# Optimization experiments

Measured on AMD Instinct MI355X. Metric: run time of the kernel, lower is better.

## Reference

```python
import jax, jax.numpy as jnp
import numpy as np

EPS = 1e-5  # torch BatchNorm default eps


def _bn(x, gamma, beta, axes):
    # training-mode batch norm over `axes` (channel axis is 1), biased variance as in torch
    mean = x.mean(axis=axes, keepdims=True)
    var = x.var(axis=axes, keepdims=True)
    shp = [1] * x.ndim
    shp[1] = -1
    return gamma.reshape(shp) * (x - mean) * jax.lax.rsqrt(var + EPS) + beta.reshape(shp)


def setup_inputs() -> dict:
    key = jax.random.key(0)
    k0, k1, k2 = jax.random.split(key, 3)
    B, C, H, W = 4, 64, 128, 128
    OP2 = 128      # out_planes * 2
    HEAD = 8       # head_dim
    HP = OP2 // HEAD  # head_planes = 16
    return {
        "x": jax.random.normal(k0, (B, C, H, W), jnp.float32),
        "w_qkv": jax.random.normal(k1, (OP2, C), jnp.float32) / np.sqrt(C).astype(np.float32),
        "gamma1": jnp.ones((OP2,), jnp.float32),
        "beta1": jnp.zeros((OP2,), jnp.float32),
        "pos_relative": jax.random.normal(k2, (HP, 2 * H - 1), jnp.float32) / np.sqrt(C).astype(np.float32),
        "gate_qr": jnp.array([0.1], jnp.float32),
        "gate_kr": jnp.array([0.1], jnp.float32),
        "gate_v_pos": jnp.array([0.1], jnp.float32),
        "gate_v": jnp.array([1.0], jnp.float32),
        "gamma_att": jnp.ones((3 * HEAD,), jnp.float32),
        "beta_att": jnp.zeros((3 * HEAD,), jnp.float32),
        "gamma_v": jnp.ones((2 * HEAD,), jnp.float32),
        "beta_v": jnp.zeros((2 * HEAD,), jnp.float32),
    }


def reference(x, w_qkv, gamma1, beta1, pos_relative, gate_qr, gate_kr,
              gate_v_pos, gate_v, gamma_att, beta_att, gamma_v, beta_v):
    b, c, H, W = x.shape
    # h_w='h': permute [0,3,1,2] -> (b, W, c, H), fuse (b, W)
    xp = jnp.transpose(x, (0, 3, 1, 2)).reshape(b * W, c, H)  # [N, c, H]
    # to_qkv: 1x1 Conv1d (no bias) + ReLU + BatchNorm1d (training mode)
    y = jax.nn.relu(jnp.einsum('oc,ncl->nol', w_qkv, xp))      # [N, 2*out_planes, H]
    y = _bn(y, gamma1, beta1, (0, 2))

    head_dim = gamma_att.shape[0] // 3
    hp = y.shape[1] // head_dim          # head_planes
    qk_dim = hp // 4
    v_dim = hp // 2
    qkv = y.reshape(-1, head_dim, hp, H)  # [N, head_dim, head_planes, H]
    q = qkv[:, :, :qk_dim]
    k = qkv[:, :, qk_dim:2 * qk_dim]
    v = qkv[:, :, 2 * qk_dim:]

    # relative-position gather: pos_relative[:, q_idx - k_idx + H - 1] -> [head_planes, H, H]
    rel = jnp.arange(H)[:, None] - jnp.arange(H)[None, :] + H - 1
    qk_pos = pos_relative[:, rel]
    q_pos = qk_pos[:qk_dim]
    k_pos = qk_pos[qk_dim:2 * qk_dim]
    v_pos = qk_pos[2 * qk_dim:]

    qk = jnp.einsum('nhcp,nhci->nhpi', q, k)                 # [N, head_dim, H, H]
    qr = jnp.einsum('nhcp,cpi->nhpi', q, q_pos) * gate_qr
    kr = jnp.einsum('nhcp,cpi->nhpi', k, k_pos) * gate_kr

    att = _bn(jnp.concatenate([qk, qr, kr], axis=1), gamma_att, beta_att, (0, 2, 3))
    att = att.reshape(-1, 3, head_dim, H, H).sum(axis=1)
    att = jax.nn.softmax(att, axis=-1)

    att_v = jnp.einsum('nhpi,nhci->nhcp', att, v * gate_v)          # [N, head_dim, v_dim, H]
    att_vp = jnp.einsum('nhpi,cpi->nhcp', att, v_pos * gate_v_pos)

    z = _bn(jnp.concatenate([att_v, att_vp], axis=1), gamma_v, beta_v, (0, 2, 3))
    z = z.reshape(b, W, 2, head_dim * v_dim, H).sum(axis=2)  # [b, W, out_planes, H]
    # h_w='h': permute [0,2,3,1] -> (b, out_planes, H, W)
    return jnp.transpose(z, (0, 2, 3, 1))
```

## Files before the change

### kernel.cpp

```cpp
#include <hip/hip_runtime.h>
#include <hip/hip_fp16.h>

#define EPS 1e-5f



typedef _Float16 half2_t __attribute__((ext_vector_type(2)));

__device__ __constant__ int pair_c [10] = {0,0,0,0,1,1,1,2,2,3};
__device__ __constant__ int pair_cp[10] = {0,1,2,3,1,2,3,2,3,3};

__device__ inline float fdot2(half2_t a, half2_t b, float c) {
#if __has_builtin(__builtin_amdgcn_fdot2)
  return __builtin_amdgcn_fdot2(a, b, c, false);
#else
  return c + (float)a[0] * (float)b[0] + (float)a[1] * (float)b[1];
#endif
}
__device__ inline half2_t bch2(unsigned u) {
  union { unsigned u; half2_t h; } x; x.u = u; return x.h;
}
__device__ inline unsigned bcu(half2_t h) {
  union { unsigned u; half2_t h; } x; x.h = h; return x.u;
}
__device__ inline unsigned packf2(float a, float b) {
  half2_t h; h[0] = (_Float16)a; h[1] = (_Float16)b;
  union { unsigned u; half2_t h; } x; x.h = h; return x.u;
}
__device__ inline unsigned pkmul(unsigned u, half2_t c) {
  return bcu(bch2(u) * c);
}

__global__ __launch_bounds__(256) void k1_gemm(
    const float* __restrict__ x, const float* __restrict__ wq,
    _Float16* __restrict__ y1h, float* __restrict__ Pbuf)
{
  __shared__ unsigned xs[32][132];
  const int b = blockIdx.x >> 7, l = blockIdx.x & 127;
  const int tid = threadIdx.x;
  const float* xp = x + (size_t)b * 1048576 + (size_t)l * 128;
  for (int idx = tid; idx < 1024; idx += 256) {
    int cp = idx >> 5, w4 = (idx & 31) * 4;
    float4 r0 = *(const float4*)&xp[(2 * cp) * 16384 + w4];
    float4 r1 = *(const float4*)&xp[(2 * cp + 1) * 16384 + w4];
    uint4 o;
    o.x = packf2(r0.x, r1.x); o.y = packf2(r0.y, r1.y);
    o.z = packf2(r0.z, r1.z); o.w = packf2(r0.w, r1.w);
    *(uint4*)&xs[cp][w4] = o;
  }
  __syncthreads();
  const int ty = tid >> 4, tx = tid & 15;
  const int o0 = ty * 8, w0 = tx * 4;
  float acc[8][8];
#pragma unroll
  for (int u = 0; u < 8; ++u)
#pragma unroll
    for (int v = 0; v < 8; ++v) acc[u][v] = 0.f;

  for (int c4 = 0; c4 < 64; c4 += 4) {
    unsigned wr[8][2];
#pragma unroll
    for (int u = 0; u < 8; ++u) {
      float4 wv = *(const float4*)&wq[(o0 + u) * 64 + c4];
      wr[u][0] = packf2(wv.x, wv.y);
      wr[u][1] = packf2(wv.z, wv.w);
    }
    const int cp0 = c4 >> 1;
#pragma unroll
    for (int d = 0; d < 2; ++d) {
      uint4 xa = *(const uint4*)&xs[cp0 + d][w0];
      uint4 xb = *(const uint4*)&xs[cp0 + d][w0 + 64];
      half2_t a0 = bch2(xa.x), a1 = bch2(xa.y), a2 = bch2(xa.z), a3 = bch2(xa.w);
      half2_t b0 = bch2(xb.x), b1 = bch2(xb.y), b2 = bch2(xb.z), b3 = bch2(xb.w);
#pragma unroll
      for (int u = 0; u < 8; ++u) {
        half2_t wh = bch2(wr[u][d]);
        acc[u][0] = fdot2(wh, a0, acc[u][0]);
        acc[u][1] = fdot2(wh, a1, acc[u][1]);
        acc[u][2] = fdot2(wh, a2, acc[u][2]);
        acc[u][3] = fdot2(wh, a3, acc[u][3]);
        acc[u][4] = fdot2(wh, b0, acc[u][4]);
        acc[u][5] = fdot2(wh, b1, acc[u][5]);
        acc[u][6] = fdot2(wh, b2, acc[u][6]);
        acc[u][7] = fdot2(wh, b3, acc[u][7]);
      }
    }
  }
  _Float16* y1p = y1h + (size_t)(b * 128 + l) * 16384;
#pragma unroll
  for (int u = 0; u < 8; ++u) {
#pragma unroll
    for (int v = 0; v < 8; ++v) acc[u][v] = fmaxf(acc[u][v], 0.f);
    uint2 pa, pb;
    pa.x = packf2(acc[u][0], acc[u][1]); pa.y = packf2(acc[u][2], acc[u][3]);
    pb.x = packf2(acc[u][4], acc[u][5]); pb.y = packf2(acc[u][6], acc[u][7]);
    *(uint2*)&y1p[(o0 + u) * 128 + w0] = pa;
    *(uint2*)&y1p[(o0 + u) * 128 + w0 + 64] = pb;
    float s  = acc[u][0] + acc[u][1] + acc[u][2] + acc[u][3]
             + acc[u][4] + acc[u][5] + acc[u][6] + acc[u][7];
    float ss = acc[u][0]*acc[u][0] + acc[u][1]*acc[u][1] + acc[u][2]*acc[u][2]
             + acc[u][3]*acc[u][3] + acc[u][4]*acc[u][4] + acc[u][5]*acc[u][5]
             + acc[u][6]*acc[u][6] + acc[u][7]*acc[u][7];
#pragma unroll
    for (int off = 1; off < 16; off <<= 1) {
      s  += __shfl_xor(s, off);
      ss += __shfl_xor(ss, off);
    }
    if (tx == 0) {
      Pbuf[blockIdx.x * 256 + o0 + u] = s;
      Pbuf[blockIdx.x * 256 + 128 + o0 + u] = ss;
    }
  }
}

__global__ __launch_bounds__(256) void k_tr(
    const _Float16* __restrict__ y1h, const float* __restrict__ Pbuf,
    const float* __restrict__ g1, const float* __restrict__ b1,
    unsigned* __restrict__ y2h)
{
  __shared__ _Float16 th[2][64][134];
  __shared__ float scsh[4];
  const int s = blockIdx.x & 63, b = blockIdx.x >> 6;
  const int h = s >> 3, slot = s & 7;
  const int o0 = 2 * s, o1 = 2 * s + 1;
  const int tid = threadIdx.x;
  {
    int r = tid >> 6, lane = tid & 63;
    int row = ((r & 1) ? o1 : o0) + (r >> 1) * 128;
    float a = 0.f;
#pragma unroll
    for (int m = 0; m < 8; ++m) a += Pbuf[(lane + 64 * m) * 256 + row];
#pragma unroll
    for (int off = 1; off < 64; off <<= 1) a += __shfl_xor(a, off);
    if (lane == 0) scsh[r] = a;
  }
  __syncthreads();
  const float inv = 1.f / 65536.f;
  const float m0 = scsh[0] * inv, v0 = scsh[2] * inv - m0 * m0;
  const float m1 = scsh[1] * inv, v1 = scsh[3] * inv - m1 * m1;
  const float sc0 = g1[o0] * rsqrtf(v0 + EPS), sh0 = b1[o0] - m0 * sc0;
  const float sc1 = g1[o1] * rsqrtf(v1 + EPS), sh1 = b1[o1] - m1 * sc1;
  for (int lh = 0; lh < 2; ++lh) {
    const int l0 = lh * 64;
    for (int idx = tid; idx < 4096; idx += 256) {
      int ll = idx >> 6, wp = idx & 63;
      size_t base = ((size_t)(b * 128 + l0 + ll) * 128) * 128 + 2 * wp;
      unsigned a0 = *(const unsigned*)&y1h[base + (size_t)o0 * 128];
      unsigned a1 = *(const unsigned*)&y1h[base + (size_t)o1 * 128];
      half2_t ha = bch2(a0), hb = bch2(a1);
      *(unsigned*)&th[0][ll][2 * wp] =
          packf2((float)ha[0] * sc0 + sh0, (float)ha[1] * sc0 + sh0);
      *(unsigned*)&th[1][ll][2 * wp] =
          packf2((float)hb[0] * sc1 + sh1, (float)hb[1] * sc1 + sh1);
    }
    __syncthreads();
    for (int idx = tid; idx < 8192; idx += 256) {
      int w = idx >> 6, ll = idx & 63;
      unsigned pk;
      { half2_t hh; hh[0] = th[0][ll][w]; hh[1] = th[1][ll][w];
        union { unsigned u; half2_t h; } xx; xx.h = hh; pk = xx.u; }
      y2h[((size_t)((b * 128 + w) * 8 + h) * 8 + slot) * 128 + l0 + ll] = pk;
    }
    __syncthreads();
  }
}

__global__ __launch_bounds__(128) void k0_pos(const float* __restrict__ pos,
                                              float* __restrict__ PT,
                                              unsigned* __restrict__ pos_h,
                                              unsigned* __restrict__ vpxg)
{
  const int blk = blockIdx.x, tid = threadIdx.x;
  if (blk == 28) {
    for (int u = tid; u < 255; u += 128) {
#pragma unroll
      for (int s = 0; s < 4; ++s)
        pos_h[u * 4 + s] = packf2(pos[(2 * s) * 255 + u], pos[(2 * s + 1) * 255 + u]);
    }
    return;
  }
  if (blk == 29) {
    for (int m = tid; m < 3084; m += 128) {
      int sel = m / 1540, rem = m - sel * 1540;
      unsigned val = 0;
      if (sel < 2 && rem < 1536) {
        int rp = rem / 12, c = rem % 12;
        if (c < 8) {
          int ua = (sel ? 254 : 253) - 2 * rp;
          int ub = ua - 1;
          float fa = (ua >= 0) ? pos[(8 + c) * 255 + ua] : 0.f;
          float fb = (ub >= 0) ? pos[(8 + c) * 255 + ub] : 0.f;
          val = packf2(fa, fb);
        }
      }
      vpxg[m] = val;
    }
    return;
  }
  __shared__ float r0[255], r1[255];
  int rowA, rowB, out;
  bool prod;
  if (blk < 4)       { rowA = blk;                 rowB = rowA;               out = blk * 128;              prod = false; }
  else if (blk < 14) { int m = blk - 4;  rowA = pair_c[m];     rowB = pair_cp[m];     out = 1024 + m * 128; prod = true; }
  else if (blk < 18) { rowA = 4 + (blk - 14);      rowB = rowA;               out = 512 + (blk - 14) * 128; prod = false; }
  else               { int m = blk - 18; rowA = 4 + pair_c[m]; rowB = 4 + pair_cp[m]; out = 2304 + m * 128; prod = true; }
  for (int u = tid; u < 255; u += 128) {
    r0[u] = pos[rowA * 255 + u];
    r1[u] = pos[rowB * 255 + u];
  }
  __syncthreads();
  float s = 0.f;
  if (prod) {
    for (int d = 0; d < 128; ++d) s += r0[tid + d] * r1[tid + d];
  } else {
    for (int d = 0; d < 128; ++d) s += r0[tid + d];
  }
  PT[out + tid] = s;
}

__global__ __launch_bounds__(256) void k3_stats(
    const unsigned* __restrict__ y2h, const float* __restrict__ PT,
    float* __restrict__ Pb3)
{
  const int W = blockIdx.x * 4 + (threadIdx.x >> 6);
  const int lane = threadIdx.x & 63;
  const unsigned* yb = y2h + (size_t)W * 1024;
  float q[4][2], k[4][2];
#pragma unroll
  for (int pl = 0; pl < 2; ++pl) {
    half2_t ha = bch2(yb[pl * 128 + lane]);
    half2_t hb = bch2(yb[pl * 128 + 64 + lane]);
    q[2 * pl][0] = (float)ha[0]; q[2 * pl + 1][0] = (float)ha[1];
    q[2 * pl][1] = (float)hb[0]; q[2 * pl + 1][1] = (float)hb[1];
    half2_t hc = bch2(yb[(2 + pl) * 128 + lane]);
    half2_t hd = bch2(yb[(2 + pl) * 128 + 64 + lane]);
    k[2 * pl][0] = (float)hc[0]; k[2 * pl + 1][0] = (float)hc[1];
    k[2 * pl][1] = (float)hd[0]; k[2 * pl + 1][1] = (float)hd[1];
  }
  float vals[32];
#pragma unroll
  for (int c = 0; c < 4; ++c) {
    vals[c]     = q[c][0] + q[c][1];
    vals[4 + c] = k[c][0] + k[c][1];
  }
#pragma unroll
  for (int m = 0; m < 10; ++m) {
    int c = pair_c[m], cp = pair_cp[m];
    vals[8 + m]  = q[c][0] * q[cp][0] + q[c][1] * q[cp][1];
    vals[18 + m] = k[c][0] * k[cp][0] + k[c][1] * k[cp][1];
  }
  float qr = 0, qrss = 0, kr = 0, krss = 0;
#pragma unroll
  for (int c = 0; c < 4; ++c) {
    qr += q[c][0] * PT[c * 128 + lane]       + q[c][1] * PT[c * 128 + 64 + lane];
    kr += k[c][0] * PT[512 + c * 128 + lane] + k[c][1] * PT[512 + c * 128 + 64 + lane];
  }
#pragma unroll
  for (int m = 0; m < 10; ++m) {
    int c = pair_c[m], cp = pair_cp[m];
    float mult = (c == cp) ? 1.f : 2.f;
    qrss += mult * (q[c][0] * q[cp][0] * PT[1024 + m * 128 + lane]
                  + q[c][1] * q[cp][1] * PT[1024 + m * 128 + 64 + lane]);
    krss += mult * (k[c][0] * k[cp][0] * PT[2304 + m * 128 + lane]
                  + k[c][1] * k[cp][1] * PT[2304 + m * 128 + 64 + lane]);
  }
  vals[28] = qr; vals[29] = qrss; vals[30] = kr; vals[31] = krss;
#pragma unroll
  for (int v = 0; v < 32; ++v) {
    float t = vals[v];
#pragma unroll
    for (int off = 1; off < 64; off <<= 1) t += __shfl_xor(t, off);
    vals[v] = t;
  }
  if (lane == 0) {
    float qk_sum = 0, qk_ss = 0;
#pragma unroll
    for (int c = 0; c < 4; ++c) qk_sum += vals[c] * vals[4 + c];
#pragma unroll
    for (int m = 0; m < 10; ++m) {
      float mult = (pair_c[m] == pair_cp[m]) ? 1.f : 2.f;
      qk_ss += mult * vals[8 + m] * vals[18 + m];
    }
    float* o = Pb3 + W * 6;
    o[0] = qk_sum; o[1] = qk_ss;
    o[2] = vals[28]; o[3] = vals[29]; o[4] = vals[30]; o[5] = vals[31];
  }
}

__global__ __launch_bounds__(384) void kR1(
    const float* __restrict__ Pb3, float* __restrict__ S,
    const float* __restrict__ ga, const float* __restrict__ ba,
    const float* __restrict__ gqr, const float* __restrict__ gkr)
{
  __shared__ float sums[48];
  const int t = threadIdx.x;
  const int col = t >> 3, sub = t & 7;
  if (col < 48) {
    const int h = col / 6, k = col % 6;
    float v = 0.f;
#pragma unroll
    for (int j = 0; j < 64; ++j) {
      int n = sub * 64 + j;
      v += Pb3[(size_t)(n * 8 + h) * 6 + k];
    }
    v += __shfl_xor(v, 1);
    v += __shfl_xor(v, 2);
    v += __shfl_xor(v, 4);
    if (sub == 0) sums[col] = v;
  }
  __syncthreads();
  if (t < 8) {
    const int h = t;
    const float inv = 1.f / 8388608.f;
    float gates[3] = {1.f, gqr[0], gkr[0]};
    float csum = 0.f;
#pragma unroll
    for (int g = 0; g < 3; ++g) {
      float mr = sums[h * 6 + 2 * g] * inv;
      float er = sums[h * 6 + 2 * g + 1] * inv;
      float gt = gates[g];
      float mean = gt * mr;
      float var = gt * gt * er - mean * mean;
      float sc = ga[g * 8 + h] * rsqrtf(var + EPS);
      S[560 + g * 8 + h] = gt * sc;
      csum += ba[g * 8 + h] - mean * sc;
    }
    S[584 + h] = csum;
  }
}

__global__ __launch_bounds__(512, 6) void k5_apply(
    const unsigned* __restrict__ y2h, const unsigned* __restrict__ pos_h,
    const unsigned* __restrict__ vpxg,
    float* __restrict__ S, _Float16* __restrict__ av, _Float16* __restrict__ avp,
    const float* __restrict__ gv_p, const float* __restrict__ gvp_p,
    float* __restrict__ Vbuf)
{
  __shared__ __align__(16) unsigned qkv_s[128][12];
  __shared__ __align__(8)  unsigned posq[256][2];
  __shared__ __align__(8)  unsigned posk[256][2];
  __shared__ __align__(16) unsigned vt[64][12];
  __shared__ __align__(16) unsigned vpxf[3084];
  __shared__ float red[8][4];
  const int h = blockIdx.x & 7, n = blockIdx.x >> 3;
  const int tid = threadIdx.x;
  const unsigned* yb = y2h + (size_t)(n * 8 + h) * 1024;
  const float C0 = S[560 + h], C1 = S[568 + h], C2 = S[576 + h], C3v = S[584 + h];
  half2_t C0h, C1h, C2h;
  C0h[0] = C0h[1] = (_Float16)C0;
  C1h[0] = C1h[1] = (_Float16)C1;
  C2h[0] = C2h[1] = (_Float16)C2;
  {
    int l = tid >> 2, s = tid & 3;
    if (s == 0) {
      unsigned q01 = yb[l], q23 = yb[128 + l];
      qkv_s[l][0] = pkmul(q01, C0h); qkv_s[l][1] = pkmul(q23, C0h);
    } else if (s == 1) {
      unsigned q01 = yb[l], q23 = yb[128 + l];
      qkv_s[l][2] = pkmul(q01, C1h); qkv_s[l][3] = pkmul(q23, C1h);
    } else if (s == 2) {
      qkv_s[l][4] = yb[256 + l]; qkv_s[l][5] = yb[384 + l];
    } else {
      qkv_s[l][6] = pkmul(yb[256 + l], C2h); qkv_s[l][7] = pkmul(yb[384 + l], C2h);
    }
  }
  if (tid < 255) {
    uint4 t4 = *(const uint4*)&pos_h[tid * 4];
    posq[tid][0] = t4.x; posq[tid][1] = t4.y;
    posk[tid][0] = t4.z; posk[tid][1] = t4.w;
  }
  for (int m = tid; m < 3084; m += 512) vpxf[m] = vpxg[m];
  if (tid < 256) {
    int s = tid & 3, jp = tid >> 2;
    unsigned a0 = yb[(4 + s) * 128 + 2 * jp];
    unsigned a1 = yb[(4 + s) * 128 + 2 * jp + 1];
    vt[jp][2 * s]     = (a0 & 0xffffu) | (a1 << 16);
    vt[jp][2 * s + 1] = (a0 >> 16) | (a1 & 0xffff0000u);
  }
  __syncthreads();

  const int p = tid >> 2, isub = tid & 3;
  uint4 qown = *(const uint4*)&qkv_s[p][0];
  uint2 kco  = *(const uint2*)&qkv_s[p][6];
  const half2_t qa01 = bch2(qown.x), qa23 = bch2(qown.y);
  const half2_t qb01 = bch2(qown.z), qb23 = bch2(qown.w);
  const half2_t kc01 = bch2(kco.x),  kc23 = bch2(kco.y);
  const unsigned* vprow = &vpxf[(p & 1) * 1540 + (63 - (p >> 1)) * 12];
  const half2_t one2 = bch2(packf2(1.f, 1.f));

  float mcur = -1e30f;
  float sum = 0.f;
  float accv[8], accvp[8];
#pragma unroll
  for (int c = 0; c < 8; ++c) { accv[c] = 0.f; accvp[c] = 0.f; }

#pragma unroll
  for (int jj = 0; jj < 8; ++jj) {
    const int jpA = isub + 8 * jj;
    const int jpB = jpA + 4;
    const int i0A = 2 * jpA, i0B = 2 * jpB;
    const int uA = p - i0A + 127;
    const int uB = uA - 8;
    uint2 kaA = *(const uint2*)&qkv_s[i0A][4];
    uint2 kbA = *(const uint2*)&qkv_s[i0A + 1][4];
    uint2 kaB = *(const uint2*)&qkv_s[i0B][4];
    uint2 kbB = *(const uint2*)&qkv_s[i0B + 1][4];
    uint2 pqA  = *(const uint2*)&posq[uA][0];
    uint2 pqA1 = *(const uint2*)&posq[uA - 1][0];
    uint2 pqB  = *(const uint2*)&posq[uB][0];
    uint2 pqB1 = *(const uint2*)&posq[uB - 1][0];
    uint2 pkA  = *(const uint2*)&posk[uA][0];
    uint2 pkA1 = *(const uint2*)&posk[uA - 1][0];
    uint2 pkB  = *(const uint2*)&posk[uB][0];
    uint2 pkB1 = *(const uint2*)&posk[uB - 1][0];
    float s0 = fdot2(qa01, bch2(kaA.x), fdot2(qa23, bch2(kaA.y),
               fdot2(qb01, bch2(pqA.x), fdot2(qb23, bch2(pqA.y),
               fdot2(kc01, bch2(pkA.x), fdot2(kc23, bch2(pkA.y), C3v))))));
    float s1 = fdot2(qa01, bch2(kbA.x), fdot2(qa23, bch2(kbA.y),
               fdot2(qb01, bch2(pqA1.x), fdot2(qb23, bch2(pqA1.y),
               fdot2(kc01, bch2(pkA1.x), fdot2(kc23, bch2(pkA1.y), C3v))))));
    float s2 = fdot2(qa01, bch2(kaB.x), fdot2(qa23, bch2(kaB.y),
               fdot2(qb01, bch2(pqB.x), fdot2(qb23, bch2(pqB.y),
               fdot2(kc01, bch2(pkB.x), fdot2(kc23, bch2(pkB.y), C3v))))));
    float s3 = fdot2(qa01, bch2(kbB.x), fdot2(qa23, bch2(kbB.y),
               fdot2(qb01, bch2(pqB1.x), fdot2(qb23, bch2(pqB1.y),
               fdot2(kc01, bch2(pkB1.x), fdot2(kc23, bch2(pkB1.y), C3v))))));
    float mp = fmaxf(fmaxf(s0, s1), fmaxf(s2, s3));
    if (mp > mcur) {
      float r = __expf(mcur - mp);
      mcur = mp;
      sum *= r;
#pragma unroll
      for (int c = 0; c < 8; ++c) { accv[c] *= r; accvp[c] *= r; }
    }
    float e0 = __expf(s0 - mcur);
    float e1 = __expf(s1 - mcur);
    float e2f = __expf(s2 - mcur);
    float e3f = __expf(s3 - mcur);
    const half2_t eA = bch2(packf2(e0, e1));
    const half2_t eB = bch2(packf2(e2f, e3f));
    sum = fdot2(eB, one2, fdot2(eA, one2, sum));
    uint4 vaA = *(const uint4*)&vt[jpA][0];
    uint4 vbA = *(const uint4*)&vt[jpA][4];
    uint4 vaB = *(const uint4*)&vt[jpB][0];
    uint4 vbB = *(const uint4*)&vt[jpB][4];
    const unsigned* wrA = vprow + jpA * 12;
    const unsigned* wrB = vprow + jpB * 12;
    uint4 waA = *(const uint4*)wrA;
    uint4 wbA = *(const uint4*)(wrA + 4);
    uint4 waB = *(const uint4*)wrB;
    uint4 wbB = *(const uint4*)(wrB + 4);
    accv[0] = fdot2(eB, bch2(vaB.x), fdot2(eA, bch2(vaA.x), accv[0]));
    accv[1] = fdot2(eB, bch2(vaB.y), fdot2(eA, bch2(vaA.y), accv[1]));
    accv[2] = fdot2(eB, bch2(vaB.z), fdot2(eA, bch2(vaA.z), accv[2]));
    accv[3] = fdot2(eB, bch2(vaB.w), fdot2(eA, bch2(vaA.w), accv[3]));
    accv[4] = fdot2(eB, bch2(vbB.x), fdot2(eA, bch2(vbA.x), accv[4]));
    accv[5] = fdot2(eB, bch2(vbB.y), fdot2(eA, bch2(vbA.y), accv[5]));
    accv[6] = fdot2(eB, bch2(vbB.z), fdot2(eA, bch2(vbA.z), accv[6]));
    accv[7] = fdot2(eB, bch2(vbB.w), fdot2(eA, bch2(vbA.w), accv[7]));
    accvp[0] = fdot2(eB, bch2(waB.x), fdot2(eA, bch2(waA.x), accvp[0]));
    accvp[1] = fdot2(eB, bch2(waB.y), fdot2(eA, bch2(waA.y), accvp[1]));
    accvp[2] = fdot2(eB, bch2(waB.z), fdot2(eA, bch2(waA.z), accvp[2]));
    accvp[3] = fdot2(eB, bch2(waB.w), fdot2(eA, bch2(waA.w), accvp[3]));
    accvp[4] = fdot2(eB, bch2(wbB.x), fdot2(eA, bch2(wbA.x), accvp[4]));
    accvp[5] = fdot2(eB, bch2(wbB.y), fdot2(eA, bch2(wbA.y), accvp[5]));
    accvp[6] = fdot2(eB, bch2(wbB.z), fdot2(eA, bch2(wbA.z), accvp[6]));
    accvp[7] = fdot2(eB, bch2(wbB.w), fdot2(eA, bch2(wbA.w), accvp[7]));
  }
  float M = fmaxf(mcur, __shfl_xor(mcur, 1));
  M = fmaxf(M, __shfl_xor(M, 2));
  {
    float r = __expf(mcur - M);
    sum *= r;
#pragma unroll
    for (int c = 0; c < 8; ++c) { accv[c] *= r; accvp[c] *= r; }
  }
  sum += __shfl_xor(sum, 1);
  sum += __shfl_xor(sum, 2);
#pragma unroll
  for (int c = 0; c < 8; ++c) {
    accv[c]  += __shfl_xor(accv[c], 1);  accv[c]  += __shfl_xor(accv[c], 2);
    accvp[c] += __shfl_xor(accvp[c], 1); accvp[c] += __shfl_xor(accvp[c], 2);
  }

  float sv = 0, ssv = 0, svp = 0, ssvp = 0;
  if (isub == 0) {
    const float fv = gv_p[0] / sum, fp2 = gvp_p[0] / sum;
    size_t base = ((size_t)(n * 8 + h) * 8) * 128 + p;
#pragma unroll
    for (int c = 0; c < 8; ++c) {
      float x1 = accv[c] * fv;
      float x2 = accvp[c] * fp2;
      av [base + c * 128] = (_Float16)x1;
      avp[base + c * 128] = (_Float16)x2;
      sv += x1; ssv += x1 * x1; svp += x2; ssvp += x2 * x2;
    }
  }
  float vals[4] = {sv, ssv, svp, ssvp};
#pragma unroll
  for (int kk = 0; kk < 4; ++kk) {
    float v = vals[kk];
#pragma unroll
    for (int off = 1; off < 64; off <<= 1) v += __shfl_xor(v, off);
    vals[kk] = v;
  }
  const int wid = tid >> 6, lane = tid & 63;
  if (lane == 0) {
#pragma unroll
    for (int kk = 0; kk < 4; ++kk) red[wid][kk] = vals[kk];
  }
  __syncthreads();
  if (tid == 0) {
    float t0 = 0, t1 = 0, t2 = 0, t3 = 0;
#pragma unroll
    for (int w = 0; w < 8; ++w) {
      t0 += red[w][0]; t1 += red[w][1]; t2 += red[w][2]; t3 += red[w][3];
    }
    float* o = Vbuf + (size_t)blockIdx.x * 4;
    o[0] = t0; o[1] = t1; o[2] = t2; o[3] = t3;
  }
}

__global__ __launch_bounds__(512) void kR2(
    const float* __restrict__ Vbuf, float* __restrict__ S,
    const float* __restrict__ gv, const float* __restrict__ bv)
{
  __shared__ float part[32][17];
  const int t = threadIdx.x;
  const int col = t >> 4, sub = t & 15;
  const int k = col >> 3, h = col & 7;
  float v = 0.f;
  for (int m = 0; m < 32; ++m) {
    int n = sub + 16 * m;
    v += Vbuf[(size_t)(n * 8 + h) * 4 + k];
  }
  part[col][sub] = v;
  __syncthreads();
  if (t < 32) {
    float s = 0.f;
#pragma unroll
    for (int j = 0; j < 16; ++j) s += part[t][j];
    part[t][16] = s;
  }
  __syncthreads();
  if (t < 8) {
    const int hh = t;
    const float inv = 1.f / 524288.f;
    float m1 = part[0 * 8 + hh][16] * inv;
    float e1 = part[1 * 8 + hh][16] * inv;
    float var = e1 - m1 * m1;
    float sc = gv[hh] * rsqrtf(var + EPS);
    S[624 + hh] = sc;
    S[632 + hh] = bv[hh] - m1 * sc;
    float m2 = part[2 * 8 + hh][16] * inv;
    float e2 = part[3 * 8 + hh][16] * inv;
    var = e2 - m2 * m2;
    sc = gv[8 + hh] * rsqrtf(var + EPS);
    S[640 + hh] = sc;
    S[648 + hh] = bv[8 + hh] - m2 * sc;
  }
}

__global__ __launch_bounds__(256) void k7_out(
    const _Float16* __restrict__ av, const _Float16* __restrict__ avp,
    const float* __restrict__ S, float* __restrict__ out)
{
  __shared__ float tile[64][129];
  const int wt = blockIdx.x & 1;
  const int d  = (blockIdx.x >> 1) & 63;
  const int b  = blockIdx.x >> 7;
  const int h = d >> 3, c = d & 7;
  const float scv = S[624 + h], shv = S[632 + h];
  const float scp = S[640 + h], shp = S[648 + h];
  const int tid = threadIdx.x;
  for (int idx = tid; idx < 8192; idx += 256) {
    int wl = idx >> 7, pp = idx & 127;
    int n = b * 128 + wt * 64 + wl;
    size_t base = (((size_t)n * 8 + h) * 8 + c) * 128 + pp;
    tile[wl][pp] = (float)av[base] * scv + shv + (float)avp[base] * scp + shp;
  }
  __syncthreads();
  for (int idx = tid; idx < 8192; idx += 256) {
    int pp = idx >> 6, wl = idx & 63;
    out[(((size_t)b * 64 + d) * 128 + pp) * 128 + wt * 64 + wl] = tile[wl][pp];
  }
}

extern "C" void kernel_launch(void* const* d_in, const int* in_sizes, int n_in,
                              void* d_out, int out_size, void* d_ws, size_t ws_size,
                              hipStream_t stream)
{
  const float* x   = (const float*)d_in[0];
  const float* wq  = (const float*)d_in[1];
  const float* g1  = (const float*)d_in[2];
  const float* b1  = (const float*)d_in[3];
  const float* pos = (const float*)d_in[4];
  const float* gqr = (const float*)d_in[5];
  const float* gkr = (const float*)d_in[6];
  const float* gvp = (const float*)d_in[7];
  const float* gv  = (const float*)d_in[8];
  const float* ga  = (const float*)d_in[9];
  const float* ba  = (const float*)d_in[10];
  const float* gv2 = (const float*)d_in[11];
  const float* bv2 = (const float*)d_in[12];

  float* ws = (float*)d_ws;
  _Float16* y1h   = (_Float16*)ws;
  _Float16* av    = (_Float16*)ws;
  _Float16* avp   = (_Float16*)ws + 4194304;
  float*    Pb3   = ws + 4200000;
  float*    Vbuf  = ws + 4250000;
  float*    Pbuf  = ws + 4300000;
  unsigned* y2h   = (unsigned*)(ws + 8388608);
  float*    S     = ws + 16777216;
  unsigned* pos_h = (unsigned*)(ws + 16778240);
  float*    PT    = ws + 16781312;
  unsigned* vpxg  = (unsigned*)(ws + 16785000);
  float*    out   = (float*)d_out;

  k0_pos<<<30, 128, 0, stream>>>(pos, PT, pos_h, vpxg);
  k1_gemm<<<512, 256, 0, stream>>>(x, wq, y1h, Pbuf);
  k_tr<<<256, 256, 0, stream>>>(y1h, Pbuf, g1, b1, y2h);
  k3_stats<<<1024, 256, 0, stream>>>(y2h, PT, Pb3);
  kR1<<<1, 384, 0, stream>>>(Pb3, S, ga, ba, gqr, gkr);
  k5_apply<<<4096, 512, 0, stream>>>(y2h, pos_h, vpxg, S, av, avp, gv, gvp, Vbuf);
  kR2<<<1, 512, 0, stream>>>(Vbuf, S, gv2, bv2);
  k7_out<<<512, 256, 0, stream>>>(av, avp, S, out);
}
```

Baseline: 177.4 us.

## Compute two query rows per thread in attention apply kernel

Halves the k5_apply block to 256 threads, with each thread now handling two adjacent query positions instead of one. The two rows share the key, value and relative-position loads from shared memory, since the position indices for adjacent rows overlap. Output is written as packed half pairs. This roughly doubles accumulator registers per thread and lowers the occupancy hint, which may limit latency hiding.

```diff
diff --git a/kernel.cpp b/kernel.cpp
--- a/kernel.cpp
+++ b/kernel.cpp
@@ -329,7 +329,7 @@
   }
 }
 
-__global__ __launch_bounds__(512, 6) void k5_apply(
+__global__ __launch_bounds__(256, 5) void k5_apply(
     const unsigned* __restrict__ y2h, const unsigned* __restrict__ pos_h,
     const unsigned* __restrict__ vpxg,
     float* __restrict__ S, _Float16* __restrict__ av, _Float16* __restrict__ avp,
@@ -341,7 +341,7 @@
   __shared__ __align__(8)  unsigned posk[256][2];
   __shared__ __align__(16) unsigned vt[64][12];
   __shared__ __align__(16) unsigned vpxf[3084];
-  __shared__ float red[8][4];
+  __shared__ float red[4][4];
   const int h = blockIdx.x & 7, n = blockIdx.x >> 3;
   const int tid = threadIdx.x;
   const unsigned* yb = y2h + (size_t)(n * 8 + h) * 1024;
@@ -350,8 +350,8 @@
   C0h[0] = C0h[1] = (_Float16)C0;
   C1h[0] = C1h[1] = (_Float16)C1;
   C2h[0] = C2h[1] = (_Float16)C2;
-  {
-    int l = tid >> 2, s = tid & 3;
+  for (int t = tid; t < 512; t += 256) {
+    int l = t >> 2, s = t & 3;
     if (s == 0) {
       unsigned q01 = yb[l], q23 = yb[128 + l];
       qkv_s[l][0] = pkmul(q01, C0h); qkv_s[l][1] = pkmul(q23, C0h);
@@ -369,8 +369,8 @@
     posq[tid][0] = t4.x; posq[tid][1] = t4.y;
     posk[tid][0] = t4.z; posk[tid][1] = t4.w;
   }
-  for (int m = tid; m < 3084; m += 512) vpxf[m] = vpxg[m];
-  if (tid < 256) {
+  for (int m = tid; m < 3084; m += 256) vpxf[m] = vpxg[m];
+  {
     int s = tid & 3, jp = tid >> 2;
     unsigned a0 = yb[(4 + s) * 128 + 2 * jp];
     unsigned a1 = yb[(4 + s) * 128 + 2 * jp + 1];
@@ -379,20 +379,29 @@
   }
   __syncthreads();
 
-  const int p = tid >> 2, isub = tid & 3;
-  uint4 qown = *(const uint4*)&qkv_s[p][0];
-  uint2 kco  = *(const uint2*)&qkv_s[p][6];
-  const half2_t qa01 = bch2(qown.x), qa23 = bch2(qown.y);
-  const half2_t qb01 = bch2(qown.z), qb23 = bch2(qown.w);
-  const half2_t kc01 = bch2(kco.x),  kc23 = bch2(kco.y);
-  const unsigned* vprow = &vpxf[(p & 1) * 1540 + (63 - (p >> 1)) * 12];
+  const int ph2 = tid >> 2, isub = tid & 3;
+  const int p = 2 * ph2;
+  uint4 qo0 = *(const uint4*)&qkv_s[p][0];
+  uint2 kc0 = *(const uint2*)&qkv_s[p][6];
+  uint4 qo1 = *(const uint4*)&qkv_s[p + 1][0];
+  uint2 kc1 = *(const uint2*)&qkv_s[p + 1][6];
+  const half2_t qa01_0 = bch2(qo0.x), qa23_0 = bch2(qo0.y);
+  const half2_t qb01_0 = bch2(qo0.z), qb23_0 = bch2(qo0.w);
+  const half2_t kc01_0 = bch2(kc0.x), kc23_0 = bch2(kc0.y);
+  const half2_t qa01_1 = bch2(qo1.x), qa23_1 = bch2(qo1.y);
+  const half2_t qb01_1 = bch2(qo1.z), qb23_1 = bch2(qo1.w);
+  const half2_t kc01_1 = bch2(kc1.x), kc23_1 = bch2(kc1.y);
+  const unsigned* vprow0 = &vpxf[(63 - ph2) * 12];
+  const unsigned* vprow1 = &vpxf[1540 + (63 - ph2) * 12];
   const half2_t one2 = bch2(packf2(1.f, 1.f));
 
-  float mcur = -1e30f;
-  float sum = 0.f;
-  float accv[8], accvp[8];
-#pragma unroll
-  for (int c = 0; c < 8; ++c) { accv[c] = 0.f; accvp[c] = 0.f; }
+  float mcur0 = -1e30f, mcur1 = -1e30f;
+  float sum0 = 0.f, sum1 = 0.f;
+  float accv0[8], accvp0[8], accv1[8], accvp1[8];
+#pragma unroll
+  for (int c = 0; c < 8; ++c) {
+    accv0[c] = 0.f; accvp0[c] = 0.f; accv1[c] = 0.f; accvp1[c] = 0.f;
+  }
 
 #pragma unroll
   for (int jj = 0; jj < 8; ++jj) {
@@ -405,95 +414,148 @@
     uint2 kbA = *(const uint2*)&qkv_s[i0A + 1][4];
     uint2 kaB = *(const uint2*)&qkv_s[i0B][4];
     uint2 kbB = *(const uint2*)&qkv_s[i0B + 1][4];
-    uint2 pqA  = *(const uint2*)&posq[uA][0];
+    uint2 pqAp = *(const uint2*)&posq[uA + 1][0];
+    uint2 pqA0 = *(const uint2*)&posq[uA][0];
     uint2 pqA1 = *(const uint2*)&posq[uA - 1][0];
-    uint2 pqB  = *(const uint2*)&posq[uB][0];
+    uint2 pqBp = *(const uint2*)&posq[uB + 1][0];
+    uint2 pqB0 = *(const uint2*)&posq[uB][0];
     uint2 pqB1 = *(const uint2*)&posq[uB - 1][0];
-    uint2 pkA  = *(const uint2*)&posk[uA][0];
+    uint2 pkAp = *(const uint2*)&posk[uA + 1][0];
+    uint2 pkA0 = *(const uint2*)&posk[uA][0];
     uint2 pkA1 = *(const uint2*)&posk[uA - 1][0];
-    uint2 pkB  = *(const uint2*)&posk[uB][0];
+    uint2 pkBp = *(const uint2*)&posk[uB + 1][0];
+    uint2 pkB0 = *(const uint2*)&posk[uB][0];
     uint2 pkB1 = *(const uint2*)&posk[uB - 1][0];
-    float s0 = fdot2(qa01, bch2(kaA.x), fdot2(qa23, bch2(kaA.y),
-               fdot2(qb01, bch2(pqA.x), fdot2(qb23, bch2(pqA.y),
-               fdot2(kc01, bch2(pkA.x), fdot2(kc23, bch2(pkA.y), C3v))))));
-    float s1 = fdot2(qa01, bch2(kbA.x), fdot2(qa23, bch2(kbA.y),
-               fdot2(qb01, bch2(pqA1.x), fdot2(qb23, bch2(pqA1.y),
-               fdot2(kc01, bch2(pkA1.x), fdot2(kc23, bch2(pkA1.y), C3v))))));
-    float s2 = fdot2(qa01, bch2(kaB.x), fdot2(qa23, bch2(kaB.y),
-               fdot2(qb01, bch2(pqB.x), fdot2(qb23, bch2(pqB.y),
-               fdot2(kc01, bch2(pkB.x), fdot2(kc23, bch2(pkB.y), C3v))))));
-    float s3 = fdot2(qa01, bch2(kbB.x), fdot2(qa23, bch2(kbB.y),
-               fdot2(qb01, bch2(pqB1.x), fdot2(qb23, bch2(pqB1.y),
-               fdot2(kc01, bch2(pkB1.x), fdot2(kc23, bch2(pkB1.y), C3v))))));
-    float mp = fmaxf(fmaxf(s0, s1), fmaxf(s2, s3));
-    if (mp > mcur) {
-      float r = __expf(mcur - mp);
-      mcur = mp;
-      sum *= r;
-#pragma unroll
-      for (int c = 0; c < 8; ++c) { accv[c] *= r; accvp[c] *= r; }
-    }
-    float e0 = __expf(s0 - mcur);
-    float e1 = __expf(s1 - mcur);
-    float e2f = __expf(s2 - mcur);
-    float e3f = __expf(s3 - mcur);
-    const half2_t eA = bch2(packf2(e0, e1));
-    const half2_t eB = bch2(packf2(e2f, e3f));
-    sum = fdot2(eB, one2, fdot2(eA, one2, sum));
+    float s0 = fdot2(qa01_0, bch2(kaA.x), fdot2(qa23_0, bch2(kaA.y),
+               fdot2(qb01_0, bch2(pqA0.x), fdot2(qb23_0, bch2(pqA0.y),
+               fdot2(kc01_0, bch2(pkA0.x), fdot2(kc23_0, bch2(pkA0.y), C3v))))));
+    float s1 = fdot2(qa01_0, bch2(kbA.x), fdot2(qa23_0, bch2(kbA.y),
+               fdot2(qb01_0, bch2(pqA1.x), fdot2(qb23_0, bch2(pqA1.y),
+               fdot2(kc01_0, bch2(pkA1.x), fdot2(kc23_0, bch2(pkA1.y), C3v))))));
+    float s2 = fdot2(qa01_0, bch2(kaB.x), fdot2(qa23_0, bch2(kaB.y),
+               fdot2(qb01_0, bch2(pqB0.x), fdot2(qb23_0, bch2(pqB0.y),
+               fdot2(kc01_0, bch2(pkB0.x), fdot2(kc23_0, bch2(pkB0.y), C3v))))));
+    float s3 = fdot2(qa01_0, bch2(kbB.x), fdot2(qa23_0, bch2(kbB.y),
+               fdot2(qb01_0, bch2(pqB1.x), fdot2(qb23_0, bch2(pqB1.y),
+               fdot2(kc01_0, bch2(pkB1.x), fdot2(kc23_0, bch2(pkB1.y), C3v))))));
+    float t0 = fdot2(qa01_1, bch2(kaA.x), fdot2(qa23_1, bch2(kaA.y),
+               fdot2(qb01_1, bch2(pqAp.x), fdot2(qb23_1, bch2(pqAp.y),
+               fdot2(kc01_1, bch2(pkAp.x), fdot2(kc23_1, bch2(pkAp.y), C3v))))));
+    float t1 = fdot2(qa01_1, bch2(kbA.x), fdot2(qa23_1, bch2(kbA.y),
+               fdot2(qb01_1, bch2(pqA0.x), fdot2(qb23_1, bch2(pqA0.y),
+               fdot2(kc01_1, bch2(pkA0.x), fdot2(kc23_1, bch2(pkA0.y), C3v))))));
+    float t2 = fdot2(qa01_1, bch2(kaB.x), fdot2(qa23_1, bch2(kaB.y),
+               fdot2(qb01_1, bch2(pqBp.x), fdot2(qb23_1, bch2(pqBp.y),
+               fdot2(kc01_1, bch2(pkBp.x), fdot2(kc23_1, bch2(pkBp.y), C3v))))));
+    float t3 = fdot2(qa01_1, bch2(kbB.x), fdot2(qa23_1, bch2(kbB.y),
+               fdot2(qb01_1, bch2(pqB0.x), fdot2(qb23_1, bch2(pqB0.y),
+               fdot2(kc01_1, bch2(pkB0.x), fdot2(kc23_1, bch2(pkB0.y), C3v))))));
+    float mp0 = fmaxf(fmaxf(s0, s1), fmaxf(s2, s3));
+    if (mp0 > mcur0) {
+      float r = __expf(mcur0 - mp0);
+      mcur0 = mp0;
+      sum0 *= r;
+#pragma unroll
+      for (int c = 0; c < 8; ++c) { accv0[c] *= r; accvp0[c] *= r; }
+    }
+    float mp1 = fmaxf(fmaxf(t0, t1), fmaxf(t2, t3));
+    if (mp1 > mcur1) {
+      float r = __expf(mcur1 - mp1);
+      mcur1 = mp1;
+      sum1 *= r;
+#pragma unroll
+      for (int c = 0; c < 8; ++c) { accv1[c] *= r; accvp1[c] *= r; }
+    }
+    float e0 = __expf(s0 - mcur0), e1 = __expf(s1 - mcur0);
+    float e2 = __expf(s2 - mcur0), e3 = __expf(s3 - mcur0);
+    float f0 = __expf(t0 - mcur1), f1 = __expf(t1 - mcur1);
+    float f2 = __expf(t2 - mcur1), f3 = __expf(t3 - mcur1);
+    const half2_t eA0 = bch2(packf2(e0, e1)), eB0 = bch2(packf2(e2, e3));
+    const half2_t eA1 = bch2(packf2(f0, f1)), eB1 = bch2(packf2(f2, f3));
+    sum0 = fdot2(eB0, one2, fdot2(eA0, one2, sum0));
+    sum1 = fdot2(eB1, one2, fdot2(eA1, one2, sum1));
     uint4 vaA = *(const uint4*)&vt[jpA][0];
     uint4 vbA = *(const uint4*)&vt[jpA][4];
     uint4 vaB = *(const uint4*)&vt[jpB][0];
     uint4 vbB = *(const uint4*)&vt[jpB][4];
-    const unsigned* wrA = vprow + jpA * 12;
-    const unsigned* wrB = vprow + jpB * 12;
-    uint4 waA = *(const uint4*)wrA;
-    uint4 wbA = *(const uint4*)(wrA + 4);
-    uint4 waB = *(const uint4*)wrB;
-    uint4 wbB = *(const uint4*)(wrB + 4);
-    accv[0] = fdot2(eB, bch2(vaB.x), fdot2(eA, bch2(vaA.x), accv[0]));
-    accv[1] = fdot2(eB, bch2(vaB.y), fdot2(eA, bch2(vaA.y), accv[1]));
-    accv[2] = fdot2(eB, bch2(vaB.z), fdot2(eA, bch2(vaA.z), accv[2]));
-    accv[3] = fdot2(eB, bch2(vaB.w), fdot2(eA, bch2(vaA.w), accv[3]));
-    accv[4] = fdot2(eB, bch2(vbB.x), fdot2(eA, bch2(vbA.x), accv[4]));
-    accv[5] = fdot2(eB, bch2(vbB.y), fdot2(eA, bch2(vbA.y), accv[5]));
-    accv[6] = fdot2(eB, bch2(vbB.z), fdot2(eA, bch2(vbA.z), accv[6]));
-    accv[7] = fdot2(eB, bch2(vbB.w), fdot2(eA, bch2(vbA.w), accv[7]));
-    accvp[0] = fdot2(eB, bch2(waB.x), fdot2(eA, bch2(waA.x), accvp[0]));
-    accvp[1] = fdot2(eB, bch2(waB.y), fdot2(eA, bch2(waA.y), accvp[1]));
-    accvp[2] = fdot2(eB, bch2(waB.z), fdot2(eA, bch2(waA.z), accvp[2]));
-    accvp[3] = fdot2(eB, bch2(waB.w), fdot2(eA, bch2(waA.w), accvp[3]));
-    accvp[4] = fdot2(eB, bch2(wbB.x), fdot2(eA, bch2(wbA.x), accvp[4]));
-    accvp[5] = fdot2(eB, bch2(wbB.y), fdot2(eA, bch2(wbA.y), accvp[5]));
-    accvp[6] = fdot2(eB, bch2(wbB.z), fdot2(eA, bch2(wbA.z), accvp[6]));
-    accvp[7] = fdot2(eB, bch2(wbB.w), fdot2(eA, bch2(wbA.w), accvp[7]));
-  }
-  float M = fmaxf(mcur, __shfl_xor(mcur, 1));
-  M = fmaxf(M, __shfl_xor(M, 2));
+    const unsigned* wrA0 = vprow0 + jpA * 12;
+    const unsigned* wrB0 = vprow0 + jpB * 12;
+    const unsigned* wrA1 = vprow1 + jpA * 12;
+    const unsigned* wrB1 = vprow1 + jpB * 12;
+    uint4 waA0 = *(const uint4*)wrA0, wbA0 = *(const uint4*)(wrA0 + 4);
+    uint4 waB0 = *(const uint4*)wrB0, wbB0 = *(const uint4*)(wrB0 + 4);
+    uint4 waA1 = *(const uint4*)wrA1, wbA1 = *(const uint4*)(wrA1 + 4);
+    uint4 waB1 = *(const uint4*)wrB1, wbB1 = *(const uint4*)(wrB1 + 4);
+    accv0[0] = fdot2(eB0, bch2(vaB.x), fdot2(eA0, bch2(vaA.x), accv0[0]));
+    accv0[1] = fdot2(eB0, bch2(vaB.y), fdot2(eA0, bch2(vaA.y), accv0[1]));
+    accv0[2] = fdot2(eB0, bch2(vaB.z), fdot2(eA0, bch2(vaA.z), accv0[2]));
+    accv0[3] = fdot2(eB0, bch2(vaB.w), fdot2(eA0, bch2(vaA.w), accv0[3]));
+    accv0[4] = fdot2(eB0, bch2(vbB.x), fdot2(eA0, bch2(vbA.x), accv0[4]));
+    accv0[5] = fdot2(eB0, bch2(vbB.y), fdot2(eA0, bch2(vbA.y), accv0[5]));
+    accv0[6] = fdot2(eB0, bch2(vbB.z), fdot2(eA0, bch2(vbA.z), accv0[6]));
+    accv0[7] = fdot2(eB0, bch2(vbB.w), fdot2(eA0, bch2(vbA.w), accv0[7]));
+    accv1[0] = fdot2(eB1, bch2(vaB.x), fdot2(eA1, bch2(vaA.x), accv1[0]));
+    accv1[1] = fdot2(eB1, bch2(vaB.y), fdot2(eA1, bch2(vaA.y), accv1[1]));
+    accv1[2] = fdot2(eB1, bch2(vaB.z), fdot2(eA1, bch2(vaA.z), accv1[2]));
+    accv1[3] = fdot2(eB1, bch2(vaB.w), fdot2(eA1, bch2(vaA.w), accv1[3]));
+    accv1[4] = fdot2(eB1, bch2(vbB.x), fdot2(eA1, bch2(vbA.x), accv1[4]));
+    accv1[5] = fdot2(eB1, bch2(vbB.y), fdot2(eA1, bch2(vbA.y), accv1[5]));
+    accv1[6] = fdot2(eB1, bch2(vbB.z), fdot2(eA1, bch2(vbA.z), accv1[6]));
+    accv1[7] = fdot2(eB1, bch2(vbB.w), fdot2(eA1, bch2(vbA.w), accv1[7]));
+    accvp0[0] = fdot2(eB0, bch2(waB0.x), fdot2(eA0, bch2(waA0.x), accvp0[0]));
+    accvp0[1] = fdot2(eB0, bch2(waB0.y), fdot2(eA0, bch2(waA0.y), accvp0[1]));
+    accvp0[2] = fdot2(eB0, bch2(waB0.z), fdot2(eA0, bch2(waA0.z), accvp0[2]));
+    accvp0[3] = fdot2(eB0, bch2(waB0.w), fdot2(eA0, bch2(waA0.w), accvp0[3]));
+    accvp0[4] = fdot2(eB0, bch2(wbB0.x), fdot2(eA0, bch2(wbA0.x), accvp0[4]));
+    accvp0[5] = fdot2(eB0, bch2(wbB0.y), fdot2(eA0, bch2(wbA0.y), accvp0[5]));
+    accvp0[6] = fdot2(eB0, bch2(wbB0.z), fdot2(eA0, bch2(wbA0.z), accvp0[6]));
+    accvp0[7] = fdot2(eB0, bch2(wbB0.w), fdot2(eA0, bch2(wbA0.w), accvp0[7]));
+    accvp1[0] = fdot2(eB1, bch2(waB1.x), fdot2(eA1, bch2(waA1.x), accvp1[0]));
+    accvp1[1] = fdot2(eB1, bch2(waB1.y), fdot2(eA1, bch2(waA1.y), accvp1[1]));
+    accvp1[2] = fdot2(eB1, bch2(waB1.z), fdot2(eA1, bch2(waA1.z), accvp1[2]));
+    accvp1[3] = fdot2(eB1, bch2(waB1.w), fdot2(eA1, bch2(waA1.w), accvp1[3]));
+    accvp1[4] = fdot2(eB1, bch2(wbB1.x), fdot2(eA1, bch2(wbA1.x), accvp1[4]));
+    accvp1[5] = fdot2(eB1, bch2(wbB1.y), fdot2(eA1, bch2(wbA1.y), accvp1[5]));
+    accvp1[6] = fdot2(eB1, bch2(wbB1.z), fdot2(eA1, bch2(wbA1.z), accvp1[6]));
+    accvp1[7] = fdot2(eB1, bch2(wbB1.w), fdot2(eA1, bch2(wbA1.w), accvp1[7]));
+  }
+  float M0 = fmaxf(mcur0, __shfl_xor(mcur0, 1));
+  M0 = fmaxf(M0, __shfl_xor(M0, 2));
+  float M1 = fmaxf(mcur1, __shfl_xor(mcur1, 1));
+  M1 = fmaxf(M1, __shfl_xor(M1, 2));
   {
-    float r = __expf(mcur - M);
-    sum *= r;
-#pragma unroll
-    for (int c = 0; c < 8; ++c) { accv[c] *= r; accvp[c] *= r; }
-  }
-  sum += __shfl_xor(sum, 1);
-  sum += __shfl_xor(sum, 2);
+    float r0 = __expf(mcur0 - M0), r1 = __expf(mcur1 - M1);
+    sum0 *= r0; sum1 *= r1;
+#pragma unroll
+    for (int c = 0; c < 8; ++c) {
+      accv0[c] *= r0; accvp0[c] *= r0;
+      accv1[c] *= r1; accvp1[c] *= r1;
+    }
+  }
+  sum0 += __shfl_xor(sum0, 1); sum0 += __shfl_xor(sum0, 2);
+  sum1 += __shfl_xor(sum1, 1); sum1 += __shfl_xor(sum1, 2);
 #pragma unroll
   for (int c = 0; c < 8; ++c) {
-    accv[c]  += __shfl_xor(accv[c], 1);  accv[c]  += __shfl_xor(accv[c], 2);
-    accvp[c] += __shfl_xor(accvp[c], 1); accvp[c] += __shfl_xor(accvp[c], 2);
+    accv0[c]  += __shfl_xor(accv0[c], 1);  accv0[c]  += __shfl_xor(accv0[c], 2);
+    accvp0[c] += __shfl_xor(accvp0[c], 1); accvp0[c] += __shfl_xor(accvp0[c], 2);
+    accv1[c]  += __shfl_xor(accv1[c], 1);  accv1[c]  += __shfl_xor(accv1[c], 2);
+    accvp1[c] += __shfl_xor(accvp1[c], 1); accvp1[c] += __shfl_xor(accvp1[c], 2);
   }
 
   float sv = 0, ssv = 0, svp = 0, ssvp = 0;
   if (isub == 0) {
-    const float fv = gv_p[0] / sum, fp2 = gvp_p[0] / sum;
+    const float gvv = gv_p[0], gvpv = gvp_p[0];
+    const float fv0 = gvv / sum0, fp0 = gvpv / sum0;
+    const float fv1 = gvv / sum1, fp1 = gvpv / sum1;
     size_t base = ((size_t)(n * 8 + h) * 8) * 128 + p;
 #pragma unroll
     for (int c = 0; c < 8; ++c) {
-      float x1 = accv[c] * fv;
-      float x2 = accvp[c] * fp2;
-      av [base + c * 128] = (_Float16)x1;
-      avp[base + c * 128] = (_Float16)x2;
-      sv += x1; ssv += x1 * x1; svp += x2; ssvp += x2 * x2;
+      float a0 = accv0[c] * fv0,  a1 = accv1[c] * fv1;
+      float b0 = accvp0[c] * fp0, b1 = accvp1[c] * fp1;
+      *(unsigned*)&av [base + c * 128] = packf2(a0, a1);
+      *(unsigned*)&avp[base + c * 128] = packf2(b0, b1);
+      sv += a0 + a1; ssv += a0 * a0 + a1 * a1;
+      svp += b0 + b1; ssvp += b0 * b0 + b1 * b1;
     }
   }
   float vals[4] = {sv, ssv, svp, ssvp};
@@ -513,7 +575,7 @@
   if (tid == 0) {
     float t0 = 0, t1 = 0, t2 = 0, t3 = 0;
 #pragma unroll
-    for (int w = 0; w < 8; ++w) {
+    for (int w = 0; w < 4; ++w) {
       t0 += red[w][0]; t1 += red[w][1]; t2 += red[w][2]; t3 += red[w][3];
     }
     float* o = Vbuf + (size_t)blockIdx.x * 4;
@@ -623,7 +685,7 @@
   k_tr<<<256, 256, 0, stream>>>(y1h, Pbuf, g1, b1, y2h);
   k3_stats<<<1024, 256, 0, stream>>>(y2h, PT, Pb3);
   kR1<<<1, 384, 0, stream>>>(Pb3, S, ga, ba, gqr, gkr);
-  k5_apply<<<4096, 512, 0, stream>>>(y2h, pos_h, vpxg, S, av, avp, gv, gvp, Vbuf);
+  k5_apply<<<4096, 256, 0, stream>>>(y2h, pos_h, vpxg, S, av, avp, gv, gvp, Vbuf);
   kR2<<<1, 512, 0, stream>>>(Vbuf, S, gv2, bv2);
   k7_out<<<512, 256, 0, stream>>>(av, avp, S, out);
 }
```

Measured after the change: 589.0 us. +232.0%, slower.
